# Performance work log

Hardware: AMD Instinct MI355X
Metric: run time of the kernel (lower is better)

The kernel has to match this reference:

```python
import jax, jax.numpy as jnp
import numpy as np

NEG = -1e30          # stand-in for -inf that is safe in fp arithmetic
EPS = 1e-7           # keras.backend.epsilon()

B, T, C, L = 64, 1024, 128, 256
BLANK = C - 1        # keras ctc_batch_cost uses last class as blank


def setup_inputs() -> dict:
    key = jax.random.key(0)
    k1, k2, k3 = jax.random.split(key, 3)
    # ctc_batch_cost expects softmax probabilities, not logits
    y_pred = jax.nn.softmax(jax.random.normal(k1, (B, T, C), dtype=jnp.float32), axis=-1)
    y_true = jax.random.randint(k2, (B, L), 0, C - 1).astype(jnp.int32)  # labels exclude blank
    input_length = jnp.full((B, 1), T, dtype=jnp.int32)
    label_length = jax.random.randint(k3, (B, 1), 1, L + 1).astype(jnp.int32)
    return {"y_true": y_true, "y_pred": y_pred,
            "input_length": input_length, "label_length": label_length}


def _logsumexp3(a, b, c):
    m = jnp.maximum(a, jnp.maximum(b, c))
    return m + jnp.log(jnp.exp(a - m) + jnp.exp(b - m) + jnp.exp(c - m))


def _ctc_loss(y_pred, y_true, input_length, label_length):
    log_probs = jnp.log(y_pred + EPS)                       # [B,T,C]
    S = 2 * L + 1
    # extended label sequence: blank, l0, blank, l1, ..., blank
    ext = jnp.full((B, S), BLANK, dtype=jnp.int32).at[:, 1::2].set(y_true)
    lab_len = label_length[:, 0]                            # [B]
    s_idx = jnp.arange(S)
    valid_s = s_idx[None, :] < (2 * lab_len + 1)[:, None]   # [B,S]
    # skip (s-2 -> s) allowed only for non-blank, non-repeated symbols
    skip_ok = jnp.concatenate(
        [jnp.zeros((B, 2), bool),
         (ext[:, 2:] != BLANK) & (ext[:, 2:] != ext[:, :-2])], axis=1)
    # gather per-extended-position log-probs: [B,T,S]
    lp_ext = jnp.take_along_axis(log_probs, jnp.broadcast_to(ext[:, None, :], (B, T, S)), axis=2)

    alpha0 = jnp.full((B, S), NEG, dtype=log_probs.dtype)
    alpha0 = alpha0.at[:, 0].set(lp_ext[:, 0, 0])
    alpha0 = alpha0.at[:, 1].set(jnp.where(lab_len > 0, lp_ext[:, 0, 1], NEG))
    alpha0 = jnp.where(valid_s, alpha0, NEG)

    def step(alpha, inp):
        lp_t, t = inp                                       # lp_t: [B,S]
        shift1 = jnp.pad(alpha[:, :-1], ((0, 0), (1, 0)), constant_values=NEG)
        shift2 = jnp.pad(alpha[:, :-2], ((0, 0), (2, 0)), constant_values=NEG)
        shift2 = jnp.where(skip_ok, shift2, NEG)
        new = _logsumexp3(alpha, shift1, shift2) + lp_t
        new = jnp.where(valid_s, new, NEG)
        # freeze alpha past each sample's input_length
        new = jnp.where(t < input_length, new, alpha)
        return new, None

    lp_tmaj = jnp.swapaxes(lp_ext, 0, 1)                    # [T,B,S]
    alpha, _ = jax.lax.scan(step, alpha0, (lp_tmaj[1:], jnp.arange(1, T)))

    end_blank = jnp.take_along_axis(alpha, (2 * lab_len)[:, None], axis=1)[:, 0]
    end_label = jnp.take_along_axis(alpha, jnp.maximum(2 * lab_len - 1, 0)[:, None], axis=1)[:, 0]
    end_label = jnp.where(lab_len > 0, end_label, NEG)
    loss = -jnp.logaddexp(end_blank, end_label)             # [B]
    return loss[:, None]                                    # (batch, 1) like ctc_batch_cost


def reference(y_true, y_pred, input_length, label_length):
    return _ctc_loss(y_pred, y_true, input_length, label_length)
```

## Files before the change

kernel.cpp:

```cpp
#include <hip/hip_runtime.h>


#define Bc 64
#define Tc 1024
#define Cc 128
#define Lc 256
#define Sc 513
#define BLANKc 127
#define CHUNK 32
#define NW 4
#define PADS 64
#define WSSTRIDE 1028

constexpr float EPSF = 1e-7f;

#define DPPMAXI(x, ctrl) max(x, __builtin_amdgcn_update_dpp( \
    0, x, ctrl, 0xf, 0xf, true))

__device__ __forceinline__ double dpp_wave_shr1_f64(double x) {
    union { double d; int i[2]; } u, r;
    u.d = x;
    r.i[0] = __builtin_amdgcn_update_dpp(0, u.i[0], 0x138, 0xf, 0xf, true);
    r.i[1] = __builtin_amdgcn_update_dpp(0, u.i[1], 0x138, 0xf, 0xf, true);
    return r.d;
}
__device__ __forceinline__ double dpp_wave_shl1_f64(double x) {
    union { double d; int i[2]; } u, r;
    u.d = x;
    r.i[0] = __builtin_amdgcn_update_dpp(0, u.i[0], 0x130, 0xf, 0xf, true);
    r.i[1] = __builtin_amdgcn_update_dpp(0, u.i[1], 0x130, 0xf, 0xf, true);
    return r.d;
}

__global__ __launch_bounds__(256) void ctc_fb_kernel(
    const int* __restrict__ y_true,
    const float* __restrict__ y_pred,
    const int* __restrict__ label_length,
    double* __restrict__ ws)
{
    const int bb = blockIdx.x;
    const int b = bb >> 1;
    const bool isF = !(bb & 1);
    const int tid = (int)threadIdx.x;
    const int wl = tid >> 6;
    const int lane = tid & 63;

    __shared__ float bufs[3][CHUNK * Cc];
    __shared__ double ash[Sc];
    __shared__ int em[NW];

    const int lab_len = label_length[b];
    const float* yp = y_pred + (size_t)b * Tc * Cc;
    const int* lab = y_true + b * Lc;
    double* wsb = ws + (size_t)b * WSSTRIDE;

    const int start = isF ? ((wl == 0) ? 0 : (128 * wl - PADS)) : (128 * wl);
    const int own_s = 128 * wl;
    const int own_e = (wl == NW - 1) ? Sc : (128 * (wl + 1));
    const int s0 = start + 4 * lane;

    const int li0 = s0 >> 1;
    const int li0c = min(li0, Lc - 1);
    const int li1c = min(li0 + 1, Lc - 1);
    const int li2c = min(li0 + 2, Lc - 1);
    const int ca = lab[li0c], cb = lab[li1c], cc = lab[li2c];
    const double sm_a = (li0 > 0 && ca != BLANKc && ca != lab[li0c - 1]) ? 1.0 : 0.0;
    const double sm_b = (cb != BLANKc && cb != ca) ? 1.0 : 0.0;
    const double sm_c = (cc != BLANKc && cc != cb) ? 1.0 : 0.0;

    const int S2 = 2 * lab_len + 1;
    const bool ow0 = (s0     >= own_s) && (s0     < own_e);
    const bool ow1 = (s0 + 1 >= own_s) && (s0 + 1 < own_e);
    const bool ow2 = (s0 + 2 >= own_s) && (s0 + 2 < own_e);
    const bool ow3 = (s0 + 3 >= own_s) && (s0 + 3 < own_e);
    const int om0 = (ow0 && s0     < S2) ? -1 : 0;
    const int om1 = (ow1 && s0 + 1 < S2) ? -1 : 0;
    const int om2 = (ow2 && s0 + 2 < S2) ? -1 : 0;
    const int om3 = (ow3 && s0 + 3 < S2) ? -1 : 0;

    auto stage = [&](int c, float* dst) {
        const float* g = yp + (size_t)c * (CHUNK * Cc) + lane * 4;
        #pragma unroll
        for (int q = 0; q < 4; ++q) {
            const int i = wl * 4 + q;
            __builtin_amdgcn_global_load_lds(
                (const __attribute__((address_space(1))) void*)(g + i * 256),
                (__attribute__((address_space(3))) void*)(dst + i * 256),
                16, 0, 0);
        }
    };

    if (isF) {
        double a0 = 0, a1 = 0, a2 = 0, a3 = 0, n3 = 0;
        int tote = 0;
        double Eb, Ea, Ec;
        double Ob, Oa, Oc;
        float sl[4][6];

        auto gpair = [&](const float* rowp, float* s) {
            s[0] = rowp[BLANKc]; s[1] = rowp[BLANKc + Cc];
            s[2] = rowp[ca];     s[3] = rowp[ca + Cc];
            s[4] = rowp[cb];     s[5] = rowp[cb + Cc];
        };
        auto expandE = [&](const float* s) {
            Eb = (double)(s[0] + EPSF); Ea = (double)(s[2] + EPSF);
            Ec = (double)(s[4] + EPSF);
        };
        auto expandO = [&](const float* s) {
            Ob = (double)(s[1] + EPSF); Oa = (double)(s[3] + EPSF);
            Oc = (double)(s[5] + EPSF);
        };
        auto stepE = [&]() {
            const double t3 = __fma_rn(sm_b, a1, a3 + a2);
            const double t2 = a2 + a1;
            const double t1 = __fma_rn(sm_a, n3, a1 + a0);
            const double t0 = a0 + n3;
            a3 = t3 * Ec;
            n3 = dpp_wave_shr1_f64(a3);
            a2 = t2 * Eb; a1 = t1 * Ea; a0 = t0 * Eb;
        };
        auto stepO = [&]() {
            const double t3 = __fma_rn(sm_b, a1, a3 + a2);
            const double t2 = a2 + a1;
            const double t1 = __fma_rn(sm_a, n3, a1 + a0);
            const double t0 = a0 + n3;
            a3 = t3 * Oc;
            n3 = dpp_wave_shr1_f64(a3);
            a2 = t2 * Ob; a1 = t1 * Oa; a0 = t0 * Ob;
        };
        auto syncex = [&](int sk) {
            int e =        om0 & (__double2hiint(a0) >> 20);
            e = max(e, om1 & (__double2hiint(a1) >> 20));
            e = max(e, om2 & (__double2hiint(a2) >> 20));
            e = max(e, om3 & (__double2hiint(a3) >> 20));
            e = DPPMAXI(e, 0x111); e = DPPMAXI(e, 0x112);
            e = DPPMAXI(e, 0x114); e = DPPMAXI(e, 0x118);
            e = DPPMAXI(e, 0x142); e = DPPMAXI(e, 0x143);
            if (lane == 63) em[wl] = e;
            if (ow0) ash[s0]     = a0;
            if (ow1) ash[s0 + 1] = a1;
            if (ow2) ash[s0 + 2] = a2;
            if (ow3) ash[s0 + 3] = a3;
            __syncthreads();
            const int eg = max(max(em[0], em[1]), max(em[2], em[3]));
            const int sexp = min(max(2046 - eg, 1), 2045);
            const double sc = __hiloint2double(sexp << 20, 0);
            tote += 1023 - sexp;
            if (wl > 0 && lane < (PADS / 4)) {
                a0 = ash[s0];     a1 = ash[s0 + 1];
                a2 = ash[s0 + 2]; a3 = ash[s0 + 3];
            }
            a0 *= sc; a1 *= sc; a2 *= sc; a3 *= sc;
            n3 = dpp_wave_shr1_f64(a3);
            __syncthreads();
            if (sk <= 15) stage(sk, bufs[sk % 3]);
        };

        stage(0, bufs[0]); stage(1, bufs[1]); stage(2, bufs[2]);
        __syncthreads();

        if (wl == 0 && lane == 0) {
            a0 = (double)(bufs[0][BLANKc] + EPSF);
            if (lab_len > 0) a1 = (double)(bufs[0][ca] + EPSF);
        }
        gpair(bufs[0] + 2 * Cc, sl[1]);
        gpair(bufs[0] + 4 * Cc, sl[2]);
        gpair(bufs[0] + 6 * Cc, sl[3]);
        {
            const float* r1 = bufs[0] + 1 * Cc;
            Ob = (double)(r1[BLANKc] + EPSF);
            Oa = (double)(r1[ca] + EPSF);
            Oc = (double)(r1[cb] + EPSF);
        }
        expandE(sl[1]);

        stepO();
        expandO(sl[1]);

        {
            const float* rb  = bufs[0];
            const float* rbn = bufs[1];
            #pragma unroll
            for (int qi = 1; qi < 16; ++qi) {
                const int rr = 2 * qi;
                const float* nxt = (rr + 6 < CHUNK) ? (rb + (rr + 6) * Cc)
                                                    : (rbn + (rr + 6 - CHUNK) * Cc);
                gpair(nxt, sl[(qi + 3) & 3]);
                stepE();
                expandE(sl[(qi + 1) & 3]);
                stepO();
                expandO(sl[(qi + 1) & 3]);
            }
        }
        for (int k = 1; k < 16; ++k) {
            syncex(k + 2);
            const float* rb  = bufs[k % 3];
            const float* rbn = bufs[(k + 1) % 3];
            #pragma unroll
            for (int qi = 0; qi < 16; ++qi) {
                const int rr = 2 * qi;
                const float* nxt = (rr + 6 < CHUNK) ? (rb + (rr + 6) * Cc)
                                                    : (rbn + (rr + 6 - CHUNK) * Cc);
                gpair(nxt, sl[(qi + 3) & 3]);
                stepE();
                expandE(sl[(qi + 1) & 3]);
                stepO();
                expandO(sl[(qi + 1) & 3]);
            }
        }
        if (ow0) wsb[s0]     = a0;
        if (ow1) wsb[s0 + 1] = a1;
        if (ow2) wsb[s0 + 2] = a2;
        if (ow3) wsb[s0 + 3] = a3;
        if (tid == 0) wsb[513] = (double)tote;
    } else {
        double b0 = 0, b1 = 0, b2 = 0, b3 = 0, n0 = 0, n1 = 0;
        int tote = 0;
        double Eb, Ea, Ec, Ed;
        double Ob, Oa, Oc, Od;
        float sl[4][8];

        auto gpair = [&](const float* rowp, float* s) {
            s[0] = rowp[BLANKc]; s[1] = rowp[BLANKc + Cc];
            s[2] = rowp[ca];     s[3] = rowp[ca + Cc];
            s[4] = rowp[cb];     s[5] = rowp[cb + Cc];
            s[6] = rowp[cc];     s[7] = rowp[cc + Cc];
        };
        auto expandE = [&](const float* s) {
            Eb = (double)(s[0] + EPSF); Ea = (double)(s[2] + EPSF);
            Ec = (double)(s[4] + EPSF); Ed = (double)(s[6] + EPSF);
        };
        auto expandO = [&](const float* s) {
            Ob = (double)(s[1] + EPSF); Oa = (double)(s[3] + EPSF);
            Oc = (double)(s[5] + EPSF); Od = (double)(s[7] + EPSF);
        };
        auto stepBE = [&]() {
            const double x1 = Ea * b1, x2 = Eb * b2, x3 = Ec * b3, z = Ed * n1;
            const double r0 = __fma_rn(Eb, b0, x1);
            const double r1 = __fma_rn(sm_b, x3, x1 + x2);
            const double r2 = x2 + x3;
            const double r3 = __fma_rn(sm_c, z, __fma_rn(Eb, n0, x3));
            b0 = r0; b1 = r1; b2 = r2; b3 = r3;
            n0 = dpp_wave_shl1_f64(b0);
            n1 = dpp_wave_shl1_f64(b1);
        };
        auto stepBO = [&]() {
            const double x1 = Oa * b1, x2 = Ob * b2, x3 = Oc * b3, z = Od * n1;
            const double r0 = __fma_rn(Ob, b0, x1);
            const double r1 = __fma_rn(sm_b, x3, x1 + x2);
            const double r2 = x2 + x3;
            const double r3 = __fma_rn(sm_c, z, __fma_rn(Ob, n0, x3));
            b0 = r0; b1 = r1; b2 = r2; b3 = r3;
            n0 = dpp_wave_shl1_f64(b0);
            n1 = dpp_wave_shl1_f64(b1);
        };
        auto syncex = [&](int sk) {
            int e =        om0 & (__double2hiint(b0) >> 20);
            e = max(e, om1 & (__double2hiint(b1) >> 20));
            e = max(e, om2 & (__double2hiint(b2) >> 20));
            e = max(e, om3 & (__double2hiint(b3) >> 20));
            e = DPPMAXI(e, 0x111); e = DPPMAXI(e, 0x112);
            e = DPPMAXI(e, 0x114); e = DPPMAXI(e, 0x118);
            e = DPPMAXI(e, 0x142); e = DPPMAXI(e, 0x143);
            if (lane == 63) em[wl] = e;
            if (ow0) ash[s0]     = b0;
            if (ow1) ash[s0 + 1] = b1;
            if (ow2) ash[s0 + 2] = b2;
            if (ow3) ash[s0 + 3] = b3;
            __syncthreads();
            const int eg = max(max(em[0], em[1]), max(em[2], em[3]));
            const int sexp = min(max(2046 - eg, 1), 2045);
            const double sc = __hiloint2double(sexp << 20, 0);
            tote += 1023 - sexp;
            if (s0     >= own_e) b0 = (s0     < Sc) ? ash[s0]     : 0.0;
            if (s0 + 1 >= own_e) b1 = (s0 + 1 < Sc) ? ash[s0 + 1] : 0.0;
            if (s0 + 2 >= own_e) b2 = (s0 + 2 < Sc) ? ash[s0 + 2] : 0.0;
            if (s0 + 3 >= own_e) b3 = (s0 + 3 < Sc) ? ash[s0 + 3] : 0.0;
            b0 *= sc; b1 *= sc; b2 *= sc; b3 *= sc;
            n0 = dpp_wave_shl1_f64(b0);
            n1 = dpp_wave_shl1_f64(b1);
            __syncthreads();
            if (sk >= 16) stage(sk, bufs[(31 - sk) % 3]);
        };

        stage(31, bufs[0]); stage(30, bufs[1]); stage(29, bufs[2]);
        __syncthreads();

        {
            const int e0 = 2 * lab_len;
            const int e1 = (lab_len > 0) ? (2 * lab_len - 1) : e0;
            b0 = (s0     == e0 || s0     == e1) ? 1.0 : 0.0;
            b1 = (s0 + 1 == e0 || s0 + 1 == e1) ? 1.0 : 0.0;
            b2 = (s0 + 2 == e0 || s0 + 2 == e1) ? 1.0 : 0.0;
            b3 = (s0 + 3 == e0 || s0 + 3 == e1) ? 1.0 : 0.0;
            n0 = dpp_wave_shl1_f64(b0);
            n1 = dpp_wave_shl1_f64(b1);
        }
        gpair(bufs[0] + 30 * Cc, sl[3]);
        gpair(bufs[0] + 28 * Cc, sl[2]);
        gpair(bufs[0] + 26 * Cc, sl[1]);
        expandO(sl[3]);
        expandE(sl[3]);

        {
            const float* rb  = bufs[0];
            const float* rbn = bufs[1];
            #pragma unroll
            for (int j = 0; j < 16; ++j) {
                const int q = 15 - j;
                const int rr = 2 * q;
                const float* nxt = (rr - 6 >= 0) ? (rb + (rr - 6) * Cc)
                                                 : (rbn + (rr - 6 + CHUNK) * Cc);
                gpair(nxt, sl[(q + 1) & 3]);
                stepBO();
                expandO(sl[(q - 1) & 3]);
                stepBE();
                expandE(sl[(q - 1) & 3]);
            }
        }
        for (int c = 30; c >= 16; --c) {
            syncex(c - 2);
            const float* rb  = bufs[(31 - c) % 3];
            const float* rbn = bufs[(32 - c) % 3];
            #pragma unroll
            for (int j = 0; j < 16; ++j) {
                const int q = 15 - j;
                const int rr = 2 * q;
                const float* nxt = (rr - 6 >= 0) ? (rb + (rr - 6) * Cc)
                                                 : (rbn + (rr - 6 + CHUNK) * Cc);
                gpair(nxt, sl[(q + 1) & 3]);
                stepBO();
                expandO(sl[(q - 1) & 3]);
                stepBE();
                expandE(sl[(q - 1) & 3]);
            }
        }
        if (ow0) wsb[514 + s0]     = b0;
        if (ow1) wsb[514 + s0 + 1] = b1;
        if (ow2) wsb[514 + s0 + 2] = b2;
        if (ow3) wsb[514 + s0 + 3] = b3;
        if (tid == 0) wsb[1027] = (double)tote;
    }
}

__global__ __launch_bounds__(64) void ctc_combine(
    const int* __restrict__ label_length,
    const double* __restrict__ ws,
    float* __restrict__ out)
{
    const int b = blockIdx.x;
    const int lane = (int)threadIdx.x;
    const int lab_len = label_length[b];
    const int S2 = 2 * lab_len + 1;
    const double* wf = ws + (size_t)b * WSSTRIDE;
    const double* wb = wf + 514;

    int eP = 0;
    for (int s = lane; s < S2; s += 64) {
        const int ea = (__double2hiint(wf[s]) >> 20) & 0x7ff;
        const int eb = (__double2hiint(wb[s]) >> 20) & 0x7ff;
        if (ea && eb) eP = max(eP, ea + eb);
    }
    #pragma unroll
    for (int m = 1; m < 64; m <<= 1) eP = max(eP, __shfl_xor(eP, m));
    const int sh = 2046 - eP;
    int k1 = sh / 2;
    int k2 = sh - k1;
    k1 = min(max(k1, -1022), 1023);
    k2 = min(max(k2, -1022), 1023);
    const double scA = __hiloint2double((1023 + k1) << 20, 0);
    const double scB = __hiloint2double((1023 + k2) << 20, 0);
    double dot = 0.0;
    for (int s = lane; s < S2; s += 64)
        dot += (wf[s] * scA) * (wb[s] * scB);
    #pragma unroll
    for (int m = 1; m < 64; m <<= 1) dot += __shfl_xor(dot, m);
    if (lane == 0) {
        const double lt = wf[513] + wb[513] - (double)k1 - (double)k2;
        out[b] = (float)(-(log(dot) + lt * 0.6931471805599453));
    }
}

extern "C" void kernel_launch(void* const* d_in, const int* in_sizes, int n_in,
                              void* d_out, int out_size, void* d_ws, size_t ws_size,
                              hipStream_t stream) {
    const int*   y_true       = (const int*)d_in[0];
    const float* y_pred       = (const float*)d_in[1];
    const int*   label_length = (const int*)d_in[3];
    float* out = (float*)d_out;
    double* ws = (double*)d_ws;

    ctc_fb_kernel<<<2 * Bc, NW * 64, 0, stream>>>(y_true, y_pred,
                                                  label_length, ws);
    ctc_combine<<<Bc, 64, 0, stream>>>(label_length, ws, out);
}
```

Measured before the change: 117.2 us.

## Fuse combine into forward-backward kernel and hand-schedule LDS reads

Merges the separate combine kernel into the forward/backward kernel: the last-finishing block of each batch pair, detected with an atomic counter, computes the final dot product and loss. The counter is zeroed by a memset launched beforehand. The LDS gathers are rewritten as inline-asm ds_read_b32 with explicit partial lgkmcnt waits so reads can overlap the recurrence arithmetic. The backward pass derives its fourth probability by a DPP lane shift instead of an extra LDS read. This removes a launch and some LDS traffic, but adds a memset node and fragile manual waitcnt handling.

Result: slower. 128.8 us (+9.9%).

```diff
diff --git a/kernel.cpp b/kernel.cpp
--- a/kernel.cpp
+++ b/kernel.cpp
@@ -11,11 +11,24 @@
 #define NW 4
 #define PADS 64
 #define WSSTRIDE 1028
+#define FLAGS_OFF (Bc * WSSTRIDE)
 
 constexpr float EPSF = 1e-7f;
+
+#define LDS3(p) ((const __attribute__((address_space(3))) float*)(p))
 
 #define DPPMAXI(x, ctrl) max(x, __builtin_amdgcn_update_dpp( \
     0, x, ctrl, 0xf, 0xf, true))
+
+#define WAITSLOT() do {                                      \
+    asm volatile("s_waitcnt lgkmcnt(12)");                   \
+    __builtin_amdgcn_sched_barrier(0);                       \
+} while (0)
+
+#define DRAINLGKM() do {                                     \
+    asm volatile("s_waitcnt lgkmcnt(0)" ::: "memory");       \
+    __builtin_amdgcn_sched_barrier(0);                       \
+} while (0)
 
 __device__ __forceinline__ double dpp_wave_shr1_f64(double x) {
     union { double d; int i[2]; } u, r;
@@ -31,12 +44,19 @@
     r.i[1] = __builtin_amdgcn_update_dpp(0, u.i[1], 0x130, 0xf, 0xf, true);
     return r.d;
 }
-
-__global__ __launch_bounds__(256) void ctc_fb_kernel(
+__device__ __forceinline__ float dpp_wave_shl1_f32(float x) {
+    union { float f; int i; } u, r;
+    u.f = x;
+    r.i = __builtin_amdgcn_update_dpp(0, u.i, 0x130, 0xf, 0xf, true);
+    return r.f;
+}
+
+__global__ __launch_bounds__(256, 1) void ctc_fb_kernel(
     const int* __restrict__ y_true,
     const float* __restrict__ y_pred,
     const int* __restrict__ label_length,
-    double* __restrict__ ws)
+    double* __restrict__ ws,
+    float* __restrict__ out)
 {
     const int bb = blockIdx.x;
     const int b = bb >> 1;
@@ -48,6 +68,7 @@
     __shared__ float bufs[3][CHUNK * Cc];
     __shared__ double ash[Sc];
     __shared__ int em[NW];
+    __shared__ int amlast;
 
     const int lab_len = label_length[b];
     const float* yp = y_pred + (size_t)b * Tc * Cc;
@@ -90,18 +111,27 @@
         }
     };
 
+    float sl[4][6];
+
+    auto gpair = [&](const float* rowp, float* s) {
+        asm volatile(
+            "ds_read_b32 %0, %6\n\t"
+            "ds_read_b32 %1, %6 offset:512\n\t"
+            "ds_read_b32 %2, %7\n\t"
+            "ds_read_b32 %3, %7 offset:512\n\t"
+            "ds_read_b32 %4, %8\n\t"
+            "ds_read_b32 %5, %8 offset:512\n\t"
+            : "=&v"(s[0]), "=&v"(s[1]), "=&v"(s[2]),
+              "=&v"(s[3]), "=&v"(s[4]), "=&v"(s[5])
+            : "v"(LDS3(rowp + BLANKc)), "v"(LDS3(rowp + ca)),
+              "v"(LDS3(rowp + cb)));
+    };
+
     if (isF) {
         double a0 = 0, a1 = 0, a2 = 0, a3 = 0, n3 = 0;
         int tote = 0;
-        double Eb, Ea, Ec;
-        double Ob, Oa, Oc;
-        float sl[4][6];
-
-        auto gpair = [&](const float* rowp, float* s) {
-            s[0] = rowp[BLANKc]; s[1] = rowp[BLANKc + Cc];
-            s[2] = rowp[ca];     s[3] = rowp[ca + Cc];
-            s[4] = rowp[cb];     s[5] = rowp[cb + Cc];
-        };
+        double Eb, Ea, Ec, Ob, Oa, Oc;
+
         auto expandE = [&](const float* s) {
             Eb = (double)(s[0] + EPSF); Ea = (double)(s[2] + EPSF);
             Ec = (double)(s[4] + EPSF);
@@ -129,6 +159,7 @@
             a2 = t2 * Ob; a1 = t1 * Oa; a0 = t0 * Ob;
         };
         auto syncex = [&](int sk) {
+            DRAINLGKM();
             int e =        om0 & (__double2hiint(a0) >> 20);
             e = max(e, om1 & (__double2hiint(a1) >> 20));
             e = max(e, om2 & (__double2hiint(a2) >> 20));
@@ -172,6 +203,7 @@
             Oa = (double)(r1[ca] + EPSF);
             Oc = (double)(r1[cb] + EPSF);
         }
+        WAITSLOT();
         expandE(sl[1]);
 
         stepO();
@@ -187,6 +219,7 @@
                                                     : (rbn + (rr + 6 - CHUNK) * Cc);
                 gpair(nxt, sl[(qi + 3) & 3]);
                 stepE();
+                WAITSLOT();
                 expandE(sl[(qi + 1) & 3]);
                 stepO();
                 expandO(sl[(qi + 1) & 3]);
@@ -203,11 +236,13 @@
                                                     : (rbn + (rr + 6 - CHUNK) * Cc);
                 gpair(nxt, sl[(qi + 3) & 3]);
                 stepE();
+                WAITSLOT();
                 expandE(sl[(qi + 1) & 3]);
                 stepO();
                 expandO(sl[(qi + 1) & 3]);
             }
         }
+        DRAINLGKM();
         if (ow0) wsb[s0]     = a0;
         if (ow1) wsb[s0 + 1] = a1;
         if (ow2) wsb[s0 + 2] = a2;
@@ -216,23 +251,17 @@
     } else {
         double b0 = 0, b1 = 0, b2 = 0, b3 = 0, n0 = 0, n1 = 0;
         int tote = 0;
-        double Eb, Ea, Ec, Ed;
-        double Ob, Oa, Oc, Od;
-        float sl[4][8];
-
-        auto gpair = [&](const float* rowp, float* s) {
-            s[0] = rowp[BLANKc]; s[1] = rowp[BLANKc + Cc];
-            s[2] = rowp[ca];     s[3] = rowp[ca + Cc];
-            s[4] = rowp[cb];     s[5] = rowp[cb + Cc];
-            s[6] = rowp[cc];     s[7] = rowp[cc + Cc];
-        };
-        auto expandE = [&](const float* s) {
+        double Eb, Ea, Ec, Ed, Ob, Oa, Oc, Od;
+
+        auto expandEB = [&](const float* s) {
             Eb = (double)(s[0] + EPSF); Ea = (double)(s[2] + EPSF);
-            Ec = (double)(s[4] + EPSF); Ed = (double)(s[6] + EPSF);
-        };
-        auto expandO = [&](const float* s) {
+            Ec = (double)(s[4] + EPSF);
+            Ed = (double)(dpp_wave_shl1_f32(s[2]) + EPSF);
+        };
+        auto expandOB = [&](const float* s) {
             Ob = (double)(s[1] + EPSF); Oa = (double)(s[3] + EPSF);
-            Oc = (double)(s[5] + EPSF); Od = (double)(s[7] + EPSF);
+            Oc = (double)(s[5] + EPSF);
+            Od = (double)(dpp_wave_shl1_f32(s[3]) + EPSF);
         };
         auto stepBE = [&]() {
             const double x1 = Ea * b1, x2 = Eb * b2, x3 = Ec * b3, z = Ed * n1;
@@ -255,6 +284,7 @@
             n1 = dpp_wave_shl1_f64(b1);
         };
         auto syncex = [&](int sk) {
+            DRAINLGKM();
             int e =        om0 & (__double2hiint(b0) >> 20);
             e = max(e, om1 & (__double2hiint(b1) >> 20));
             e = max(e, om2 & (__double2hiint(b2) >> 20));
@@ -299,8 +329,9 @@
         gpair(bufs[0] + 30 * Cc, sl[3]);
         gpair(bufs[0] + 28 * Cc, sl[2]);
         gpair(bufs[0] + 26 * Cc, sl[1]);
-        expandO(sl[3]);
-        expandE(sl[3]);
+        WAITSLOT();
+        expandOB(sl[3]);
+        expandEB(sl[3]);
 
         {
             const float* rb  = bufs[0];
@@ -313,9 +344,10 @@
                                                  : (rbn + (rr - 6 + CHUNK) * Cc);
                 gpair(nxt, sl[(q + 1) & 3]);
                 stepBO();
-                expandO(sl[(q - 1) & 3]);
+                WAITSLOT();
+                expandOB(sl[(q - 1) & 3]);
                 stepBE();
-                expandE(sl[(q - 1) & 3]);
+                expandEB(sl[(q - 1) & 3]);
             }
         }
         for (int c = 30; c >= 16; --c) {
@@ -330,54 +362,54 @@
                                                  : (rbn + (rr - 6 + CHUNK) * Cc);
                 gpair(nxt, sl[(q + 1) & 3]);
                 stepBO();
-                expandO(sl[(q - 1) & 3]);
+                WAITSLOT();
+                expandOB(sl[(q - 1) & 3]);
                 stepBE();
-                expandE(sl[(q - 1) & 3]);
+                expandEB(sl[(q - 1) & 3]);
             }
         }
+        DRAINLGKM();
         if (ow0) wsb[514 + s0]     = b0;
         if (ow1) wsb[514 + s0 + 1] = b1;
         if (ow2) wsb[514 + s0 + 2] = b2;
         if (ow3) wsb[514 + s0 + 3] = b3;
         if (tid == 0) wsb[1027] = (double)tote;
     }
-}
-
-__global__ __launch_bounds__(64) void ctc_combine(
-    const int* __restrict__ label_length,
-    const double* __restrict__ ws,
-    float* __restrict__ out)
-{
-    const int b = blockIdx.x;
-    const int lane = (int)threadIdx.x;
-    const int lab_len = label_length[b];
-    const int S2 = 2 * lab_len + 1;
-    const double* wf = ws + (size_t)b * WSSTRIDE;
-    const double* wb = wf + 514;
-
-    int eP = 0;
-    for (int s = lane; s < S2; s += 64) {
-        const int ea = (__double2hiint(wf[s]) >> 20) & 0x7ff;
-        const int eb = (__double2hiint(wb[s]) >> 20) & 0x7ff;
-        if (ea && eb) eP = max(eP, ea + eb);
+
+    __threadfence();
+    if (tid == 0) {
+        int* flags = (int*)(ws + FLAGS_OFF);
+        amlast = (atomicAdd(&flags[b], 1) == 1);
     }
-    #pragma unroll
-    for (int m = 1; m < 64; m <<= 1) eP = max(eP, __shfl_xor(eP, m));
-    const int sh = 2046 - eP;
-    int k1 = sh / 2;
-    int k2 = sh - k1;
-    k1 = min(max(k1, -1022), 1023);
-    k2 = min(max(k2, -1022), 1023);
-    const double scA = __hiloint2double((1023 + k1) << 20, 0);
-    const double scB = __hiloint2double((1023 + k2) << 20, 0);
-    double dot = 0.0;
-    for (int s = lane; s < S2; s += 64)
-        dot += (wf[s] * scA) * (wb[s] * scB);
-    #pragma unroll
-    for (int m = 1; m < 64; m <<= 1) dot += __shfl_xor(dot, m);
-    if (lane == 0) {
-        const double lt = wf[513] + wb[513] - (double)k1 - (double)k2;
-        out[b] = (float)(-(log(dot) + lt * 0.6931471805599453));
+    __syncthreads();
+    if (amlast && tid < 64) {
+        __threadfence();
+        const double* wf = ws + (size_t)b * WSSTRIDE;
+        const double* wb = wf + 514;
+        int eP = 0;
+        for (int s = tid; s < S2; s += 64) {
+            const int ea = (__double2hiint(wf[s]) >> 20) & 0x7ff;
+            const int eb2 = (__double2hiint(wb[s]) >> 20) & 0x7ff;
+            if (ea && eb2) eP = max(eP, ea + eb2);
+        }
+        #pragma unroll
+        for (int m = 1; m < 64; m <<= 1) eP = max(eP, __shfl_xor(eP, m));
+        const int sh = 2046 - eP;
+        int k1 = sh / 2;
+        int k2 = sh - k1;
+        k1 = min(max(k1, -1022), 1023);
+        k2 = min(max(k2, -1022), 1023);
+        const double scA = __hiloint2double((1023 + k1) << 20, 0);
+        const double scB = __hiloint2double((1023 + k2) << 20, 0);
+        double dot = 0.0;
+        for (int s = tid; s < S2; s += 64)
+            dot += (wf[s] * scA) * (wb[s] * scB);
+        #pragma unroll
+        for (int m = 1; m < 64; m <<= 1) dot += __shfl_xor(dot, m);
+        if (tid == 0) {
+            const double lt = wf[513] + wb[513] - (double)k1 - (double)k2;
+            out[b] = (float)(-(log(dot) + lt * 0.6931471805599453));
+        }
     }
 }
 
@@ -390,7 +422,8 @@
     float* out = (float*)d_out;
     double* ws = (double*)d_ws;
 
+    hipMemsetAsync((char*)d_ws + FLAGS_OFF * sizeof(double), 0,
+                   Bc * sizeof(int), stream);
     ctc_fb_kernel<<<2 * Bc, NW * 64, 0, stream>>>(y_true, y_pred,
-                                                  label_length, ws);
-    ctc_combine<<<Bc, 64, 0, stream>>>(label_length, ws, out);
+                                                  label_length, ws, out);
 }
```
